# Kernel tuning notes

Hardware: AMD Instinct MI355X
Metric: run time of the kernel (lower is better)

## Reference

```python
import jax, jax.numpy as jnp
import numpy as np

B, T, S, D, H = 32, 256, 256, 512, 1024
VNT, VR = 300, 20000


def setup_inputs() -> dict:
    key = jax.random.key(0)
    ks = jax.random.split(key, 18)
    s = 0.02  # weight init scale to keep tanh/sigmoid unsaturated
    inp = {}
    inp['nt'] = jax.random.randint(ks[0], (B, T), 0, VNT)
    inp['prev_rules'] = jax.random.randint(ks[1], (B, T), 0, VR)
    inp['parent_rules'] = jax.random.randint(ks[2], (B, T), 0, VR)
    # parent timestep for each position; values >= i fall back to initial zero state slot
    inp['parent_t'] = jax.random.randint(ks[3], (B, T), 0, T)
    inp['context'] = jax.random.normal(ks[4], (B, S, H), jnp.float32)
    inp['context_lengths'] = jax.random.randint(ks[5], (B,), 1, S + 1)
    inp['h0'] = jnp.zeros((B, H), jnp.float32)
    inp['c0'] = jnp.zeros((B, H), jnp.float32)
    # embedding tables; row 0 is padding_idx -> zeroed
    inp['nt_emb'] = (jax.random.normal(ks[6], (VNT, D), jnp.float32)).at[0].set(0.0)
    inp['rule_emb'] = (jax.random.normal(ks[7], (VR, D), jnp.float32)).at[0].set(0.0)
    IN = 3 * D + H
    inp['W_ih'] = jax.random.normal(ks[8], (4 * H, IN), jnp.float32) * s
    inp['W_hh'] = jax.random.normal(ks[9], (4 * H, H), jnp.float32) * s
    inp['b_ih'] = jnp.zeros((4 * H,), jnp.float32)
    inp['b_hh'] = jnp.zeros((4 * H,), jnp.float32)
    inp['Wa_in'] = jax.random.normal(ks[10], (H, H), jnp.float32) * s
    inp['Wa_out'] = jax.random.normal(ks[11], (H, 2 * H), jnp.float32) * s
    inp['Wc_in'] = jax.random.normal(ks[12], (H, H), jnp.float32) * s
    inp['Wc_out'] = jax.random.normal(ks[13], (H, 2 * H), jnp.float32) * s
    return inp


def _forward(nt, prev_rules, parent_rules, parent_t, context, context_lengths,
             h0, c0, nt_emb, rule_emb, W_ih, W_hh, b_ih, b_hh,
             Wa_in, Wa_out, Wc_in, Wc_out):
    Bv, Tv = nt.shape
    Sv = context.shape[1]
    Hv = h0.shape[-1]
    dt = context.dtype

    nt_e = nt_emb[nt]               # [B,T,D]
    rule_e = rule_emb[prev_rules]   # [B,T,D]
    par_e = rule_emb[parent_rules]  # [B,T,D]

    src_mask = jnp.arange(Sv)[None, :] < context_lengths[:, None]  # [B,S]
    neg_inf = jnp.finfo(dt).min

    def global_attn(q, W_in, W_out):
        # OpenNMT GlobalAttention, attn_type='general', single decode step
        scores = jnp.einsum('bh,bsh->bs', q @ W_in.T, context)
        scores = jnp.where(src_mask, scores, neg_inf)
        p = jax.nn.softmax(scores, axis=-1)                 # [B,S]
        c_vec = jnp.einsum('bs,bsh->bh', p, context)        # [B,H]
        out = jnp.tanh(jnp.concatenate([c_vec, q], axis=-1) @ W_out.T)
        return out, p

    def step(carry, xs):
        h, c, buf, i = carry
        nt_i, r_i, pr_i, pidx = xs
        # gather parent hidden state; future/invalid parent -> slot 0 (initial zeros)
        idx = jnp.where(pidx < i, pidx + 1, 0)                       # [B]
        pstate = jnp.take_along_axis(buf, idx[:, None, None], axis=1)[:, 0]  # [B,H]
        x = jnp.concatenate([nt_i, r_i, pr_i, pstate], axis=-1)     # [B,3D+H]
        gates = x @ W_ih.T + h @ W_hh.T + b_ih + b_hh
        ig, fg, gg, og = jnp.split(gates, 4, axis=-1)                # torch order i,f,g,o
        c_new = jax.nn.sigmoid(fg) * c + jax.nn.sigmoid(ig) * jnp.tanh(gg)
        h_new = jax.nn.sigmoid(og) * jnp.tanh(c_new)
        a_out, a_p = global_attn(h_new, Wa_in, Wa_out)
        _, cp_p = global_attn(a_out, Wc_in, Wc_out)
        # scatter this step's rnn output into the parent-state buffer (slot i+1)
        buf = buf.at[:, i + 1, :].set(h_new)
        return (h_new, c_new, buf, i + 1), (a_out, a_p, cp_p)

    buf0 = jnp.zeros((Bv, Tv + 1, Hv), dt)
    xs = (nt_e.swapaxes(0, 1), rule_e.swapaxes(0, 1), par_e.swapaxes(0, 1),
          parent_t.swapaxes(0, 1))
    _, (outs, att, cp) = jax.lax.scan(step, (h0, c0, buf0, jnp.int32(0)), xs)
    output = outs.swapaxes(0, 1)       # [B,T,H]
    attn_scores = att.swapaxes(0, 1)   # [B,T,S]
    copy_scores = cp.swapaxes(0, 1)    # [B,T,S]
    return output, attn_scores, copy_scores


def reference(nt, prev_rules, parent_rules, parent_t, context, context_lengths,
              h0, c0, nt_emb, rule_emb, W_ih, W_hh, b_ih, b_hh,
              Wa_in, Wa_out, Wc_in, Wc_out):
    return _forward(nt, prev_rules, parent_rules, parent_t, context,
                    context_lengths, h0, c0, nt_emb, rule_emb, W_ih, W_hh,
                    b_ih, b_hh, Wa_in, Wa_out, Wc_in, Wc_out)
```

## Files before the change

kernel.cpp:

```cpp
#include <hip/hip_runtime.h>

typedef _Float16 f16;
typedef _Float16 h8 __attribute__((ext_vector_type(8)));
typedef float f4 __attribute__((ext_vector_type(4)));

#define Bn 32
#define Tn 256
#define Sn 256
#define Hn 1024
#define INn 2560
#define KT 3584
#define SW_PAD 3592
#define SLOT 32832
#define SC_PAD 17

__device__ __forceinline__ f4 mfma_f16(h8 a, h8 b, f4 c) {
  return __builtin_amdgcn_mfma_f32_16x16x32_f16(a, b, c, 0, 0, 0);
}
__device__ __forceinline__ float sigm(float x) { return 1.0f / (1.0f + __expf(-x)); }

__global__ void k_prep_weights(const float* __restrict__ W_ih, const float* __restrict__ W_hh,
                               const float* __restrict__ Wa_in, const float* __restrict__ Wc_in,
                               const float* __restrict__ Wa_out, const float* __restrict__ b_ih,
                               const float* __restrict__ b_hh,
                               f16* __restrict__ Wcomb, f16* __restrict__ Wain,
                               f16* __restrict__ Wcin, f16* __restrict__ Waout,
                               float* __restrict__ bcomb) {
  long idx = (long)blockIdx.x * 256 + threadIdx.x;
  if (idx < 14680064L) {
    int n = (int)(idx / KT), k = (int)(idx % KT);
    float v = (k < INn) ? W_ih[(long)n * INn + k] : W_hh[(long)n * Hn + (k - INn)];
    Wcomb[idx] = (f16)v;
    return;
  }
  idx -= 14680064L;
  if (idx < 1048576) { Wain[idx] = (f16)Wa_in[idx]; return; }
  idx -= 1048576;
  if (idx < 1048576) { Wcin[idx] = (f16)Wc_in[idx]; return; }
  idx -= 1048576;
  if (idx < 2097152) { Waout[idx] = (f16)Wa_out[idx]; return; }
  idx -= 2097152;
  if (idx < 4096) bcomb[idx] = b_ih[idx] + b_hh[idx];
}

__global__ void k_prep_ctx(const float* __restrict__ context,
                           f16* __restrict__ ctx16, f16* __restrict__ ctxT) {
  int idx = blockIdx.x * 256 + threadIdx.x;
  int b = idx >> 18;
  int rem = idx & 262143;
  int s = rem >> 10, k = rem & 1023;
  float v = context[idx];
  ctx16[idx] = (f16)v;
  ctxT[((long)b << 18) + ((long)k << 8) + s] = (f16)v;
}

__global__ void k_prep_xemb(const int* __restrict__ nt, const int* __restrict__ prev_r,
                            const int* __restrict__ par_r,
                            const float* __restrict__ nt_emb, const float* __restrict__ rule_emb,
                            f16* __restrict__ xemb) {
  int bt = blockIdx.x;
  int b = bt >> 8, t = bt & 255;
  int nti = nt[bt], pri = prev_r[bt], pai = par_r[bt];
  f16* dst = xemb + ((long)t * Bn + b) * 1536;
  for (int k = threadIdx.x; k < 1536; k += 256) {
    float v;
    if (k < 512)       v = nt_emb[(long)nti * 512 + k];
    else if (k < 1024) v = rule_emb[(long)pri * 512 + (k - 512)];
    else               v = rule_emb[(long)pai * 512 + (k - 1024)];
    dst[k] = (f16)v;
  }
}

__global__ void k_prep_state(f16* __restrict__ bufh, int* __restrict__ flags) {
  int idx = blockIdx.x * 256 + threadIdx.x;
  if (idx < 16384) {
    __hip_atomic_store((unsigned int*)bufh + idx, 0u, __ATOMIC_RELAXED,
                       __HIP_MEMORY_SCOPE_SYSTEM);
  } else if (idx < 16384 + 640) {
    __hip_atomic_store(flags + (idx - 16384), 0, __ATOMIC_RELAXED,
                       __HIP_MEMORY_SCOPE_SYSTEM);
  }
}

struct GatesArgs {
  const f16* xemb; const f16* Wcomb; f16* bufh; const float* bcomb;
  const float* c0; const int* parent_t; int* flags;
};

__global__ void __launch_bounds__(512, 1) k_gates(GatesArgs a) {
  const int jt = blockIdx.x;
  const int tid = threadIdx.x;
  const int wave = tid >> 6;
  const int lane = tid & 63;
  const int l15 = lane & 15, quad = lane >> 4;

  extern __shared__ char smem[];
  f16 (*sW)[SW_PAD] = (f16(*)[SW_PAD])smem;
  float* sC    = (float*)(smem + 114944);
  float* sBias = (float*)(smem + 123648);
  float* c_lds = (float*)(smem + 123712);
  f16*   sH    = (f16*)(smem + 124224);
  int*   spidx = (int*)(smem + 124480);

  for (int i = tid; i < 16 * 448; i += 512) {
    int n = i / 448, kk = (i % 448) * 8;
    int gr = (n >> 2) * Hn + jt * 4 + (n & 3);
    *(h8*)&sW[n][kk] = *(const h8*)(a.Wcomb + (long)gr * KT + kk);
  }
  if (tid < 16) sBias[tid] = a.bcomb[(tid >> 2) * Hn + jt * 4 + (tid & 3)];
  if (tid < 128) c_lds[tid] = a.c0[(tid >> 2) * Hn + jt * 4 + (tid & 3)];
  __syncthreads();

  for (int t = 0; t < Tn; ++t) {
    if (tid < 32) {
      int pt = a.parent_t[tid * Tn + t];
      spidx[tid] = (pt < t) ? pt + 1 : 0;
    }

    const f16* xr0 = a.xemb + ((long)t * Bn + l15) * 1536;
    const f16* xr1 = xr0 + 16 * 1536;
    f4 acc0 = (f4){0.f, 0.f, 0.f, 0.f}, acc1 = (f4){0.f, 0.f, 0.f, 0.f};
#pragma unroll
    for (int ks = 0; ks < 6; ++ks) {
      int k = wave * 192 + ks * 32 + quad * 8;
      h8 a0 = *(const h8*)(xr0 + k);
      h8 a1 = *(const h8*)(xr1 + k);
      h8 bf = *(const h8*)&sW[l15][k];
      acc0 = mfma_f16(a0, bf, acc0);
      acc1 = mfma_f16(a1, bf, acc1);
    }

    if (t > 0 && wave == 0) {
      if (jt == 0) {
        bool ok = false;
        do {
          int f0 = __hip_atomic_load(&a.flags[lane],       __ATOMIC_RELAXED, __HIP_MEMORY_SCOPE_SYSTEM);
          int f1 = __hip_atomic_load(&a.flags[64 + lane],  __ATOMIC_RELAXED, __HIP_MEMORY_SCOPE_SYSTEM);
          int f2 = __hip_atomic_load(&a.flags[128 + lane], __ATOMIC_RELAXED, __HIP_MEMORY_SCOPE_SYSTEM);
          int f3 = __hip_atomic_load(&a.flags[192 + lane], __ATOMIC_RELAXED, __HIP_MEMORY_SCOPE_SYSTEM);
          ok = (f0 >= t) && (f1 >= t) && (f2 >= t) && (f3 >= t);
        } while (!__all(ok));
        if (lane < 8)
          __hip_atomic_store(&a.flags[512 + lane * 16], t,
                             __ATOMIC_RELAXED, __HIP_MEMORY_SCOPE_SYSTEM);
      } else {
        const int ei = 512 + ((jt & 7) << 4);
        int e;
        do {
          e = __hip_atomic_load(&a.flags[ei], __ATOMIC_RELAXED, __HIP_MEMORY_SCOPE_SYSTEM);
        } while (e < t);
      }
    }
    __syncthreads();

    const f16* b0;
    const f16* b1;
    int koff;
    if (wave < 4) {
      int pidx0 = spidx[l15], pidx1 = spidx[16 + l15];
      b0 = a.bufh + (long)pidx0 * SLOT + (long)l15 * 1024;
      b1 = a.bufh + (long)pidx1 * SLOT + (long)(16 + l15) * 1024;
      koff = 1536;
    } else {
      b0 = a.bufh + (long)t * SLOT + (long)l15 * 1024;
      b1 = a.bufh + (long)t * SLOT + (long)(16 + l15) * 1024;
      koff = 2560;
    }
#pragma unroll
    for (int ks = 0; ks < 8; ++ks) {
      int k = 1536 + wave * 256 + ks * 32 + quad * 8;
      h8 a0 = *(const h8*)(b0 + (k - koff));
      h8 a1 = *(const h8*)(b1 + (k - koff));
      h8 bf = *(const h8*)&sW[l15][k];
      acc0 = mfma_f16(a0, bf, acc0);
      acc1 = mfma_f16(a1, bf, acc1);
    }

    float* myC0 = sC + (((wave & 3) * 2 + 0) * 16 + quad * 4) * SC_PAD + l15;
    float* myC1 = sC + (((wave & 3) * 2 + 1) * 16 + quad * 4) * SC_PAD + l15;
    if (wave < 4) {
#pragma unroll
      for (int r = 0; r < 4; ++r) { myC0[r * SC_PAD] = acc0[r]; myC1[r * SC_PAD] = acc1[r]; }
    }
    __syncthreads();
    if (wave >= 4) {
#pragma unroll
      for (int r = 0; r < 4; ++r) { myC0[r * SC_PAD] += acc0[r]; myC1[r * SC_PAD] += acc1[r]; }
    }
    __syncthreads();

    if (tid < 128) {
      int b = tid >> 2, jj = tid & 3;
      int mt = b >> 4, row = b & 15;
      float g0 = 0.f, g1 = 0.f, g2 = 0.f, g3 = 0.f;
#pragma unroll
      for (int w = 0; w < 4; ++w) {
        const float* base = sC + ((w * 2 + mt) * 16 + row) * SC_PAD + jj;
        g0 += base[0]; g1 += base[4]; g2 += base[8]; g3 += base[12];
      }
      g0 += sBias[jj]; g1 += sBias[4 + jj]; g2 += sBias[8 + jj]; g3 += sBias[12 + jj];
      float cp = c_lds[tid];
      float cn = sigm(g1) * cp + sigm(g0) * tanhf(g2);
      float hn = sigm(g3) * tanhf(cn);
      c_lds[tid] = cn;
      sH[tid] = (f16)hn;
    }
    __syncthreads();

    if (tid < 32) {
      unsigned long long v = *(const unsigned long long*)(sH + tid * 4);
      __hip_atomic_store((unsigned long long*)(a.bufh + (long)(t + 1) * SLOT
                                               + (long)tid * 1024 + jt * 4),
                         v, __ATOMIC_RELAXED, __HIP_MEMORY_SCOPE_SYSTEM);
    }
    asm volatile("s_waitcnt vmcnt(0)" ::: "memory");
    if (tid == 0)
      __hip_atomic_store(&a.flags[jt], t + 1,
                         __ATOMIC_RELAXED, __HIP_MEMORY_SCOPE_SYSTEM);
  }
}

__global__ void k_qgemm(const f16* __restrict__ A, const f16* __restrict__ W,
                        f16* __restrict__ out, int a_mode) {
  int tid = threadIdx.x, lane = tid & 63, wave = tid >> 6;
  int l15 = lane & 15, quad = lane >> 4;
  int wm = wave & 1, wn = wave >> 1;
  int bm = blockIdx.y * 64 + wm * 32, bn = blockIdx.x * 64 + wn * 32;

  const f16* arow[2]; const f16* brow[2];
#pragma unroll
  for (int i = 0; i < 2; ++i) {
    int m = bm + i * 16 + l15;
    arow[i] = a_mode ? A + (long)((m & 255) + 1) * SLOT + (long)(m >> 8) * 1024
                     : A + (long)m * 1024;
  }
#pragma unroll
  for (int j = 0; j < 2; ++j) brow[j] = W + (long)(bn + j * 16 + l15) * 1024;

  f4 acc[2][2];
#pragma unroll
  for (int i = 0; i < 2; ++i)
#pragma unroll
    for (int j = 0; j < 2; ++j) acc[i][j] = (f4){0.f, 0.f, 0.f, 0.f};

  for (int ks = 0; ks < 32; ++ks) {
    int k = ks * 32 + quad * 8;
    h8 af[2] = {*(const h8*)(arow[0] + k), *(const h8*)(arow[1] + k)};
    h8 bf[2] = {*(const h8*)(brow[0] + k), *(const h8*)(brow[1] + k)};
#pragma unroll
    for (int i = 0; i < 2; ++i)
#pragma unroll
      for (int j = 0; j < 2; ++j) acc[i][j] = mfma_f16(af[i], bf[j], acc[i][j]);
  }
#pragma unroll
  for (int i = 0; i < 2; ++i)
#pragma unroll
    for (int j = 0; j < 2; ++j)
#pragma unroll
      for (int r = 0; r < 4; ++r) {
        int m = bm + i * 16 + quad * 4 + r;
        int n = bn + j * 16 + l15;
        out[(long)m * 1024 + n] = (f16)acc[i][j][r];
      }
}

__global__ void k_scores(const f16* __restrict__ Q, const f16* __restrict__ C16,
                         float* __restrict__ outp) {
  int tid = threadIdx.x, lane = tid & 63, wave = tid >> 6;
  int l15 = lane & 15, quad = lane >> 4;
  int wm = wave & 1, wn = wave >> 1;
  int b = blockIdx.z;
  int bm = blockIdx.y * 64 + wm * 32, bn = blockIdx.x * 64 + wn * 32;
  const f16* A = Q + (long)b * 256 * 1024;
  const f16* Bp = C16 + (long)b * 256 * 1024;
  const f16* arow[2]; const f16* brow[2];
#pragma unroll
  for (int i = 0; i < 2; ++i) arow[i] = A + (long)(bm + i * 16 + l15) * 1024;
#pragma unroll
  for (int j = 0; j < 2; ++j) brow[j] = Bp + (long)(bn + j * 16 + l15) * 1024;
  f4 acc[2][2];
#pragma unroll
  for (int i = 0; i < 2; ++i)
#pragma unroll
    for (int j = 0; j < 2; ++j) acc[i][j] = (f4){0.f, 0.f, 0.f, 0.f};
  for (int ks = 0; ks < 32; ++ks) {
    int k = ks * 32 + quad * 8;
    h8 af[2] = {*(const h8*)(arow[0] + k), *(const h8*)(arow[1] + k)};
    h8 bf[2] = {*(const h8*)(brow[0] + k), *(const h8*)(brow[1] + k)};
#pragma unroll
    for (int i = 0; i < 2; ++i)
#pragma unroll
      for (int j = 0; j < 2; ++j) acc[i][j] = mfma_f16(af[i], bf[j], acc[i][j]);
  }
#pragma unroll
  for (int i = 0; i < 2; ++i)
#pragma unroll
    for (int j = 0; j < 2; ++j)
#pragma unroll
      for (int r = 0; r < 4; ++r) {
        int m = bm + i * 16 + quad * 4 + r;
        int n = bn + j * 16 + l15;
        outp[((long)b * 256 + m) * 256 + n] = acc[i][j][r];
      }
}

__global__ void k_softmax(float* __restrict__ rows, const int* __restrict__ ctx_len,
                          f16* __restrict__ pout) {
  int tid = threadIdx.x;
  long base = (long)blockIdx.x * 256;
  int b = blockIdx.x >> 8;
  int len = ctx_len[b];
  float v = rows[base + tid];
  bool valid = tid < len;
  __shared__ float red[256];
  red[tid] = valid ? v : -3.0e38f;
  __syncthreads();
  for (int o = 128; o > 0; o >>= 1) {
    if (tid < o) red[tid] = fmaxf(red[tid], red[tid + o]);
    __syncthreads();
  }
  float m = red[0];
  __syncthreads();
  float e = valid ? __expf(v - m) : 0.f;
  red[tid] = e;
  __syncthreads();
  for (int o = 128; o > 0; o >>= 1) {
    if (tid < o) red[tid] += red[tid + o];
    __syncthreads();
  }
  float p = e / red[0];
  rows[base + tid] = p;
  if (pout) pout[base + tid] = (f16)p;
}

__global__ void k_cvec(const f16* __restrict__ P, const f16* __restrict__ CT,
                       f16* __restrict__ out) {
  int tid = threadIdx.x, lane = tid & 63, wave = tid >> 6;
  int l15 = lane & 15, quad = lane >> 4;
  int wm = wave & 1, wn = wave >> 1;
  int b = blockIdx.z;
  int bm = blockIdx.y * 64 + wm * 32, bn = blockIdx.x * 64 + wn * 32;
  const f16* A = P + (long)b * 256 * 256;
  const f16* Bp = CT + (long)b * 1024 * 256;
  const f16* arow[2]; const f16* brow[2];
#pragma unroll
  for (int i = 0; i < 2; ++i) arow[i] = A + (long)(bm + i * 16 + l15) * 256;
#pragma unroll
  for (int j = 0; j < 2; ++j) brow[j] = Bp + (long)(bn + j * 16 + l15) * 256;
  f4 acc[2][2];
#pragma unroll
  for (int i = 0; i < 2; ++i)
#pragma unroll
    for (int j = 0; j < 2; ++j) acc[i][j] = (f4){0.f, 0.f, 0.f, 0.f};
  for (int ks = 0; ks < 8; ++ks) {
    int k = ks * 32 + quad * 8;
    h8 af[2] = {*(const h8*)(arow[0] + k), *(const h8*)(arow[1] + k)};
    h8 bf[2] = {*(const h8*)(brow[0] + k), *(const h8*)(brow[1] + k)};
#pragma unroll
    for (int i = 0; i < 2; ++i)
#pragma unroll
      for (int j = 0; j < 2; ++j) acc[i][j] = mfma_f16(af[i], bf[j], acc[i][j]);
  }
#pragma unroll
  for (int i = 0; i < 2; ++i)
#pragma unroll
    for (int j = 0; j < 2; ++j)
#pragma unroll
      for (int r = 0; r < 4; ++r) {
        int m = bm + i * 16 + quad * 4 + r;
        int n = bn + j * 16 + l15;
        out[((long)b * 256 + m) * 1024 + n] = (f16)acc[i][j][r];
      }
}

__global__ void k_aout(const f16* __restrict__ CV, const f16* __restrict__ bufh,
                       const f16* __restrict__ W, float* __restrict__ outf,
                       f16* __restrict__ outh) {
  int tid = threadIdx.x, lane = tid & 63, wave = tid >> 6;
  int l15 = lane & 15, quad = lane >> 4;
  int wm = wave & 1, wn = wave >> 1;
  int bm = blockIdx.y * 64 + wm * 32, bn = blockIdx.x * 64 + wn * 32;
  const f16* arow1[2]; const f16* arow2[2]; const f16* brow[2];
#pragma unroll
  for (int i = 0; i < 2; ++i) {
    int m = bm + i * 16 + l15;
    arow1[i] = CV + (long)m * 1024;
    arow2[i] = bufh + (long)((m & 255) + 1) * SLOT + (long)(m >> 8) * 1024;
  }
#pragma unroll
  for (int j = 0; j < 2; ++j) brow[j] = W + (long)(bn + j * 16 + l15) * 2048;
  f4 acc[2][2];
#pragma unroll
  for (int i = 0; i < 2; ++i)
#pragma unroll
    for (int j = 0; j < 2; ++j) acc[i][j] = (f4){0.f, 0.f, 0.f, 0.f};
  for (int ks = 0; ks < 64; ++ks) {
    int k = ks * 32 + quad * 8;
    h8 af[2], bf[2];
    if (k < 1024) {
      af[0] = *(const h8*)(arow1[0] + k);
      af[1] = *(const h8*)(arow1[1] + k);
    } else {
      af[0] = *(const h8*)(arow2[0] + (k - 1024));
      af[1] = *(const h8*)(arow2[1] + (k - 1024));
    }
    bf[0] = *(const h8*)(brow[0] + k);
    bf[1] = *(const h8*)(brow[1] + k);
#pragma unroll
    for (int i = 0; i < 2; ++i)
#pragma unroll
      for (int j = 0; j < 2; ++j) acc[i][j] = mfma_f16(af[i], bf[j], acc[i][j]);
  }
#pragma unroll
  for (int i = 0; i < 2; ++i)
#pragma unroll
    for (int j = 0; j < 2; ++j)
#pragma unroll
      for (int r = 0; r < 4; ++r) {
        int m = bm + i * 16 + quad * 4 + r;
        int n = bn + j * 16 + l15;
        float v = tanhf(acc[i][j][r]);
        outf[(long)m * 1024 + n] = v;
        outh[(long)m * 1024 + n] = (f16)v;
      }
}

extern "C" void kernel_launch(void* const* d_in, const int* in_sizes, int n_in,
                              void* d_out, int out_size, void* d_ws, size_t ws_size,
                              hipStream_t stream) {
  const int*   nt        = (const int*)d_in[0];
  const int*   prev_r    = (const int*)d_in[1];
  const int*   par_r     = (const int*)d_in[2];
  const int*   parent_t  = (const int*)d_in[3];
  const float* context   = (const float*)d_in[4];
  const int*   ctx_len   = (const int*)d_in[5];
  const float* c0        = (const float*)d_in[7];
  const float* nt_emb    = (const float*)d_in[8];
  const float* rule_emb  = (const float*)d_in[9];
  const float* W_ih      = (const float*)d_in[10];
  const float* W_hh      = (const float*)d_in[11];
  const float* b_ih      = (const float*)d_in[12];
  const float* b_hh      = (const float*)d_in[13];
  const float* Wa_in     = (const float*)d_in[14];
  const float* Wa_out    = (const float*)d_in[15];
  const float* Wc_in     = (const float*)d_in[16];
  float* out = (float*)d_out;

  char* ws = (char*)d_ws;
  f16*   bufh  = (f16*)(ws);
  f16*   xemb  = (f16*)(ws + 16875648L);
  f16*   Wcomb = (f16*)(ws + 42041472L);
  f16*   Wain  = (f16*)(ws + 71401600L);
  f16*   Wcin  = (f16*)(ws + 73498752L);
  f16*   Waout = (f16*)(ws + 75595904L);
  f16*   ctx16 = (f16*)(ws + 79790208L);
  f16*   ctxT  = (f16*)(ws + 96567424L);
  f16*   qbuf  = (f16*)(ws + 113344640L);
  f16*   pbuf  = (f16*)(ws + 130121856L);
  f16*   cvec  = (f16*)(ws + 134316160L);
  f16*   aout16= (f16*)(ws + 151093376L);
  int*   flags = (int*)(ws + 167870592L);
  float* bcomb = (float*)(ws + 167903360L);

  float* attn_out = out + 8388608;
  float* copy_out = out + 10485760;

  hipLaunchKernelGGL(k_prep_weights, dim3(73744), dim3(256), 0, stream,
                     W_ih, W_hh, Wa_in, Wc_in, Wa_out, b_ih, b_hh,
                     Wcomb, Wain, Wcin, Waout, bcomb);
  hipLaunchKernelGGL(k_prep_ctx, dim3(32768), dim3(256), 0, stream, context, ctx16, ctxT);
  hipLaunchKernelGGL(k_prep_xemb, dim3(8192), dim3(256), 0, stream,
                     nt, prev_r, par_r, nt_emb, rule_emb, xemb);
  hipLaunchKernelGGL(k_prep_state, dim3(96), dim3(256), 0, stream, bufh, flags);

  GatesArgs ga{xemb, Wcomb, bufh, bcomb, c0, parent_t, flags};
  void* gp[] = {&ga};
  hipLaunchCooperativeKernel((void*)k_gates, dim3(256), dim3(512), gp, 124608, stream);

  hipLaunchKernelGGL(k_qgemm, dim3(16, 128), dim3(256), 0, stream, bufh, Wain, qbuf, 1);
  hipLaunchKernelGGL(k_scores, dim3(4, 4, 32), dim3(256), 0, stream, qbuf, ctx16, attn_out);
  hipLaunchKernelGGL(k_softmax, dim3(8192), dim3(256), 0, stream, attn_out, ctx_len, pbuf);
  hipLaunchKernelGGL(k_cvec, dim3(16, 4, 32), dim3(256), 0, stream, pbuf, ctxT, cvec);
  hipLaunchKernelGGL(k_aout, dim3(16, 128), dim3(256), 0, stream, cvec, bufh, Waout, out, aout16);
  hipLaunchKernelGGL(k_qgemm, dim3(16, 128), dim3(256), 0, stream, aout16, Wcin, qbuf, 0);
  hipLaunchKernelGGL(k_scores, dim3(4, 4, 32), dim3(256), 0, stream, qbuf, ctx16, copy_out);
  hipLaunchKernelGGL(k_softmax, dim3(8192), dim3(256), 0, stream, copy_out, ctx_len, (f16*)nullptr);
}
```

Baseline: 2.932 ms.

## Flatten inter-block step barrier and prefetch next-step embedding loads into registers

Removes the two-level barrier, where block 0 gathered all flags and re-broadcast an epoch. Every block now polls all 256 per-block flags directly, which cuts one propagation hop per timestep but adds global polling traffic. The next timestep's embedding operands are loaded into registers during the current step, and the recurrent-state loads are batched ahead of their MFMAs to hide load latency. Launch bounds are raised to 2 blocks per CU. This caps VGPRs while register demand grows, so spilling is a risk.

```diff
diff --git a/kernel.cpp b/kernel.cpp
--- a/kernel.cpp
+++ b/kernel.cpp
@@ -76,7 +76,7 @@
   if (idx < 16384) {
     __hip_atomic_store((unsigned int*)bufh + idx, 0u, __ATOMIC_RELAXED,
                        __HIP_MEMORY_SCOPE_SYSTEM);
-  } else if (idx < 16384 + 640) {
+  } else if (idx < 16384 + 256) {
     __hip_atomic_store(flags + (idx - 16384), 0, __ATOMIC_RELAXED,
                        __HIP_MEMORY_SCOPE_SYSTEM);
   }
@@ -87,7 +87,7 @@
   const float* c0; const int* parent_t; int* flags;
 };
 
-__global__ void __launch_bounds__(512, 1) k_gates(GatesArgs a) {
+__global__ void __launch_bounds__(512, 2) k_gates(GatesArgs a) {
   const int jt = blockIdx.x;
   const int tid = threadIdx.x;
   const int wave = tid >> 6;
@@ -109,6 +109,18 @@
   }
   if (tid < 16) sBias[tid] = a.bcomb[(tid >> 2) * Hn + jt * 4 + (tid & 3)];
   if (tid < 128) c_lds[tid] = a.c0[(tid >> 2) * Hn + jt * 4 + (tid & 3)];
+
+  h8 aA[12];
+  {
+    const f16* xr0 = a.xemb + (long)l15 * 1536;
+    const f16* xr1 = xr0 + 16 * 1536;
+#pragma unroll
+    for (int ks = 0; ks < 6; ++ks) {
+      int k = wave * 192 + ks * 32 + quad * 8;
+      aA[2 * ks]     = *(const h8*)(xr0 + k);
+      aA[2 * ks + 1] = *(const h8*)(xr1 + k);
+    }
+  }
   __syncthreads();
 
   for (int t = 0; t < Tn; ++t) {
@@ -117,39 +129,24 @@
       spidx[tid] = (pt < t) ? pt + 1 : 0;
     }
 
-    const f16* xr0 = a.xemb + ((long)t * Bn + l15) * 1536;
-    const f16* xr1 = xr0 + 16 * 1536;
     f4 acc0 = (f4){0.f, 0.f, 0.f, 0.f}, acc1 = (f4){0.f, 0.f, 0.f, 0.f};
 #pragma unroll
     for (int ks = 0; ks < 6; ++ks) {
       int k = wave * 192 + ks * 32 + quad * 8;
-      h8 a0 = *(const h8*)(xr0 + k);
-      h8 a1 = *(const h8*)(xr1 + k);
       h8 bf = *(const h8*)&sW[l15][k];
-      acc0 = mfma_f16(a0, bf, acc0);
-      acc1 = mfma_f16(a1, bf, acc1);
+      acc0 = mfma_f16(aA[2 * ks], bf, acc0);
+      acc1 = mfma_f16(aA[2 * ks + 1], bf, acc1);
     }
 
     if (t > 0 && wave == 0) {
-      if (jt == 0) {
-        bool ok = false;
-        do {
-          int f0 = __hip_atomic_load(&a.flags[lane],       __ATOMIC_RELAXED, __HIP_MEMORY_SCOPE_SYSTEM);
-          int f1 = __hip_atomic_load(&a.flags[64 + lane],  __ATOMIC_RELAXED, __HIP_MEMORY_SCOPE_SYSTEM);
-          int f2 = __hip_atomic_load(&a.flags[128 + lane], __ATOMIC_RELAXED, __HIP_MEMORY_SCOPE_SYSTEM);
-          int f3 = __hip_atomic_load(&a.flags[192 + lane], __ATOMIC_RELAXED, __HIP_MEMORY_SCOPE_SYSTEM);
-          ok = (f0 >= t) && (f1 >= t) && (f2 >= t) && (f3 >= t);
-        } while (!__all(ok));
-        if (lane < 8)
-          __hip_atomic_store(&a.flags[512 + lane * 16], t,
-                             __ATOMIC_RELAXED, __HIP_MEMORY_SCOPE_SYSTEM);
-      } else {
-        const int ei = 512 + ((jt & 7) << 4);
-        int e;
-        do {
-          e = __hip_atomic_load(&a.flags[ei], __ATOMIC_RELAXED, __HIP_MEMORY_SCOPE_SYSTEM);
-        } while (e < t);
-      }
+      bool ok = false;
+      do {
+        int f0 = __hip_atomic_load(&a.flags[lane * 4 + 0], __ATOMIC_RELAXED, __HIP_MEMORY_SCOPE_SYSTEM);
+        int f1 = __hip_atomic_load(&a.flags[lane * 4 + 1], __ATOMIC_RELAXED, __HIP_MEMORY_SCOPE_SYSTEM);
+        int f2 = __hip_atomic_load(&a.flags[lane * 4 + 2], __ATOMIC_RELAXED, __HIP_MEMORY_SCOPE_SYSTEM);
+        int f3 = __hip_atomic_load(&a.flags[lane * 4 + 3], __ATOMIC_RELAXED, __HIP_MEMORY_SCOPE_SYSTEM);
+        ok = (f0 >= t) && (f1 >= t) && (f2 >= t) && (f3 >= t);
+      } while (!__all(ok));
     }
     __syncthreads();
 
@@ -166,14 +163,30 @@
       b1 = a.bufh + (long)t * SLOT + (long)(16 + l15) * 1024;
       koff = 2560;
     }
+    h8 bB[16];
 #pragma unroll
     for (int ks = 0; ks < 8; ++ks) {
       int k = 1536 + wave * 256 + ks * 32 + quad * 8;
-      h8 a0 = *(const h8*)(b0 + (k - koff));
-      h8 a1 = *(const h8*)(b1 + (k - koff));
+      bB[2 * ks]     = *(const h8*)(b0 + (k - koff));
+      bB[2 * ks + 1] = *(const h8*)(b1 + (k - koff));
+    }
+    {
+      int tp1 = (t + 1) & 255;
+      const f16* xr0 = a.xemb + ((long)tp1 * Bn + l15) * 1536;
+      const f16* xr1 = xr0 + 16 * 1536;
+#pragma unroll
+      for (int ks = 0; ks < 6; ++ks) {
+        int k = wave * 192 + ks * 32 + quad * 8;
+        aA[2 * ks]     = *(const h8*)(xr0 + k);
+        aA[2 * ks + 1] = *(const h8*)(xr1 + k);
+      }
+    }
+#pragma unroll
+    for (int ks = 0; ks < 8; ++ks) {
+      int k = 1536 + wave * 256 + ks * 32 + quad * 8;
       h8 bf = *(const h8*)&sW[l15][k];
-      acc0 = mfma_f16(a0, bf, acc0);
-      acc1 = mfma_f16(a1, bf, acc1);
+      acc0 = mfma_f16(bB[2 * ks], bf, acc0);
+      acc1 = mfma_f16(bB[2 * ks + 1], bf, acc1);
     }
 
     float* myC0 = sC + (((wave & 3) * 2 + 0) * 16 + quad * 4) * SC_PAD + l15;
```

Result: no change. 2.963 ms (+1.1%).
